# Kernel optimization log

Hardware: AMD Instinct MI355X
Metric: run time of the kernel (lower is better)

The kernel has to match this reference:

```python
import jax, jax.numpy as jnp
import numpy as np

CROP = 14          # initial_crop_size
POOL_K = 2         # maxpool_kernel_size == maxpool_stride


def setup_inputs() -> dict:
    key = jax.random.key(0)
    k1, k2 = jax.random.split(key)
    features = jax.random.normal(k1, (1, 50, 50, 1024), dtype=jnp.float32)
    raw = jax.random.uniform(k2, (1, 300, 4), dtype=jnp.float32)
    # well-formed normalized boxes: y1<=y2, x1<=x2
    ys = jnp.sort(raw[..., 0::2], axis=-1)
    xs = jnp.sort(raw[..., 1::2], axis=-1)
    boxes = jnp.stack([ys[..., 0], xs[..., 0], ys[..., 1], xs[..., 1]], axis=-1)
    return {"features": features, "boxes": boxes}


def _crop_and_resize(feat, boxes, crop_size):
    # feat: [H, W, C]; boxes: [N, 4] normalized (y1, x1, y2, x2)
    # Matches tf.image.crop_and_resize bilinear semantics for crop_size > 1.
    H, W, _ = feat.shape
    y1, x1, y2, x2 = boxes[:, 0], boxes[:, 1], boxes[:, 2], boxes[:, 3]
    grid = jnp.arange(crop_size, dtype=feat.dtype)  # [S]
    # sample coordinates in source pixel space: [N, S]
    ys = y1[:, None] * (H - 1) + grid[None, :] * ((y2 - y1) * (H - 1) / (crop_size - 1))[:, None]
    xs = x1[:, None] * (W - 1) + grid[None, :] * ((x2 - x1) * (W - 1) / (crop_size - 1))[:, None]
    y0f = jnp.floor(ys)
    x0f = jnp.floor(xs)
    wy = (ys - y0f)[:, :, None, None]  # [N, S, 1, 1]
    wx = (xs - x0f)[:, None, :, None]  # [N, 1, S, 1]
    y0 = jnp.clip(y0f.astype(jnp.int32), 0, H - 1)
    y1i = jnp.clip(y0 + 1, 0, H - 1)
    x0 = jnp.clip(x0f.astype(jnp.int32), 0, W - 1)
    x1i = jnp.clip(x0 + 1, 0, W - 1)
    # four corner gathers -> [N, S, S, C]
    tl = feat[y0[:, :, None], x0[:, None, :]]
    tr = feat[y0[:, :, None], x1i[:, None, :]]
    bl = feat[y1i[:, :, None], x0[:, None, :]]
    br = feat[y1i[:, :, None], x1i[:, None, :]]
    top = tl + (tr - tl) * wx
    bot = bl + (br - bl) * wx
    return top + (bot - top) * wy


def reference(features, boxes):
    # features: [1, H, W, C]; boxes: [1, N, 4]
    crops = _crop_and_resize(features[0], boxes[0], CROP)  # [N, 14, 14, C]
    N, S, _, C = crops.shape
    P = S // POOL_K
    # 2x2 stride-2 max pool (kernel == stride, S even)
    pooled = crops.reshape(N, P, POOL_K, P, POOL_K, C).max(axis=(2, 4))  # [N, 7, 7, C]
    return pooled[None]  # [1, N, 7, 7, C]
```

## Files before the change

### kernel.cpp

```cpp
#include <hip/hip_runtime.h>
#include <math.h>

#define FH 50
#define FW 50
#define FC 1024
#define FC4 256
#define NBOX 300
#define PO 7
#define CHQ 4
#define NPIX (FH * FW * FC)
#define BF16_BYTES (NPIX * 2)

typedef float nat4 __attribute__((ext_vector_type(4)));

__device__ __forceinline__ nat4 lerp4(nat4 a, nat4 b, float w) {
    return a + (b - a) * w;
}
__device__ __forceinline__ nat4 max4(nat4 a, nat4 b) {
    nat4 r;
    r.x = fmaxf(a.x, b.x);
    r.y = fmaxf(a.y, b.y);
    r.z = fmaxf(a.z, b.z);
    r.w = fmaxf(a.w, b.w);
    return r;
}
__device__ __forceinline__ nat4 bf2f(uint2 u) {
    nat4 r;
    r.x = __uint_as_float(u.x << 16);
    r.y = __uint_as_float(u.x & 0xffff0000u);
    r.z = __uint_as_float(u.y << 16);
    r.w = __uint_as_float(u.y & 0xffff0000u);
    return r;
}
__device__ __forceinline__ unsigned bfpack(float a, float b) {
    unsigned ua = __float_as_uint(a);
    unsigned ub = __float_as_uint(b);
    ua += 0x7fffu + ((ua >> 16) & 1u);
    ub += 0x7fffu + ((ub >> 16) & 1u);
    return (ua >> 16) | (ub & 0xffff0000u);
}

__global__ __launch_bounds__(256) void cvt_kernel(
    const float* __restrict__ feat, unsigned* __restrict__ ws)
{
    const int i = blockIdx.x * 256 + threadIdx.x;
    const float4 v = reinterpret_cast<const float4*>(feat)[i];
    uint2 w;
    w.x = bfpack(v.x, v.y);
    w.y = bfpack(v.z, v.w);
    reinterpret_cast<uint2*>(ws)[i] = w;
}

template<int NR>
__device__ __forceinline__ void pool_rows(
    const uint2* __restrict__ f2, const int (&rows)[NR], int c,
    float basex, float stepx, float wyA, float wyB,
    nat4* __restrict__ obase)
{
    uint2 cur[NR][2], nxt[NR][2];
    int cc;
    {
        const float xf = floorf(basex);
        cc = min(max((int)xf, 0), FW - 1);
        const int x1 = min(cc + 1, FW - 1);
#pragma unroll
        for (int q = 0; q < NR; ++q) {
            cur[q][0] = f2[(rows[q] + cc) * FC4 + c];
            cur[q][1] = f2[(rows[q] + x1) * FC4 + c];
        }
    }

    nat4 m = (nat4)(-INFINITY);
    for (int ix = 0; ix < 2 * PO; ++ix) {
        int d = 0;
        if (ix < 2 * PO - 1) {
            const float xsn = basex + (float)(ix + 1) * stepx;
            const int nx0 = min(max((int)floorf(xsn), 0), FW - 1);
            const int nx1 = min(nx0 + 1, FW - 1);
            d = nx0 - cc;
            if (d == 1) {
#pragma unroll
                for (int q = 0; q < NR; ++q)
                    nxt[q][1] = f2[(rows[q] + nx1) * FC4 + c];
            } else if (d >= 2) {
#pragma unroll
                for (int q = 0; q < NR; ++q) {
                    nxt[q][0] = f2[(rows[q] + nx0) * FC4 + c];
                    nxt[q][1] = f2[(rows[q] + nx1) * FC4 + c];
                }
            }
            cc = nx0;
        }

        {
            const float xs = basex + (float)ix * stepx;
            const float wx = xs - floorf(xs);
            const nat4 a0 = lerp4(bf2f(cur[0][0]), bf2f(cur[0][1]), wx);
            const nat4 a1 = lerp4(bf2f(cur[1][0]), bf2f(cur[1][1]), wx);
            const nat4 vA = lerp4(a0, a1, wyA);
            nat4 vB;
            if constexpr (NR == 2) {
                vB = lerp4(a0, a1, wyB);
            } else if constexpr (NR == 3) {
                const nat4 a2 = lerp4(bf2f(cur[2][0]), bf2f(cur[2][1]), wx);
                vB = lerp4(a1, a2, wyB);
            } else {
                const nat4 a2 = lerp4(bf2f(cur[2][0]), bf2f(cur[2][1]), wx);
                const nat4 a3 = lerp4(bf2f(cur[3][0]), bf2f(cur[3][1]), wx);
                vB = lerp4(a2, a3, wyB);
            }
            m = max4(m, max4(vA, vB));
        }

        if (ix & 1) {
            __builtin_nontemporal_store(m, obase + (ix >> 1) * FC4);
            m = (nat4)(-INFINITY);
        }

        if (ix < 2 * PO - 1) {
            if (d == 1) {
#pragma unroll
                for (int q = 0; q < NR; ++q) { cur[q][0] = cur[q][1]; cur[q][1] = nxt[q][1]; }
            } else if (d >= 2) {
#pragma unroll
                for (int q = 0; q < NR; ++q) { cur[q][0] = nxt[q][0]; cur[q][1] = nxt[q][1]; }
            }
        }
    }
}

__global__ __launch_bounds__(256) void roi_pool_bf16_kernel(
    const unsigned* __restrict__ ws,
    const float* __restrict__ boxes,
    float* __restrict__ out)
{
    const int j = blockIdx.x & 7;
    const int k = blockIdx.x >> 3;
    const int n = j + 8 * (k / PO);
    if (n >= NBOX) return;
    const int py = k % PO;
    const int c  = threadIdx.x;

    const float by1 = boxes[n * 4 + 0];
    const float bx1 = boxes[n * 4 + 1];
    const float by2 = boxes[n * 4 + 2];
    const float bx2 = boxes[n * 4 + 3];

    const float stepy = (by2 - by1) * (49.0f / 13.0f);
    const float stepx = (bx2 - bx1) * (49.0f / 13.0f);
    const float basey = by1 * 49.0f;
    const float basex = bx1 * 49.0f;

    const float ysA = basey + (float)(2 * py) * stepy;
    const float ysB = ysA + stepy;
    const float fA = floorf(ysA); const float wyA = ysA - fA;
    const float fB = floorf(ysB); const float wyB = ysB - fB;
    const int y0A = min(max((int)fA, 0), FH - 1); const int y1A = min(y0A + 1, FH - 1);
    const int y0B = min(max((int)fB, 0), FH - 1); const int y1B = min(y0B + 1, FH - 1);

    const uint2* __restrict__ f2 = reinterpret_cast<const uint2*>(ws);
    nat4* __restrict__ obase =
        reinterpret_cast<nat4*>(out) + (size_t)(n * (PO * PO) + py * PO) * FC4 + c;

    if (y0B == y0A) {
        const int rows[2] = {y0A * FW, y1A * FW};
        pool_rows<2>(f2, rows, c, basex, stepx, wyA, wyB, obase);
    } else if (y0B == y1A) {
        const int rows[3] = {y0A * FW, y1A * FW, y1B * FW};
        pool_rows<3>(f2, rows, c, basex, stepx, wyA, wyB, obase);
    } else {
        const int rows[4] = {y0A * FW, y1A * FW, y0B * FW, y1B * FW};
        pool_rows<4>(f2, rows, c, basex, stepx, wyA, wyB, obase);
    }
}

__global__ __launch_bounds__(64) void roi_pool_f32_kernel(
    const float* __restrict__ feat,
    const float* __restrict__ boxes,
    float* __restrict__ out)
{
    const int j = blockIdx.x & 7;
    const int k = blockIdx.x >> 3;
    const int n = j + 8 * (k / (PO * CHQ));
    if (n >= NBOX) return;
    const int r  = k % (PO * CHQ);
    const int py = r >> 2;
    const int cq = r & 3;
    const int c4 = cq * 64 + threadIdx.x;

    const float by1 = boxes[n * 4 + 0];
    const float bx1 = boxes[n * 4 + 1];
    const float by2 = boxes[n * 4 + 2];
    const float bx2 = boxes[n * 4 + 3];
    const float stepy = (by2 - by1) * (49.0f / 13.0f);
    const float stepx = (bx2 - bx1) * (49.0f / 13.0f);
    const float basey = by1 * 49.0f;
    const float basex = bx1 * 49.0f;
    const float ysA = basey + (float)(2 * py) * stepy;
    const float ysB = ysA + stepy;
    const float fA = floorf(ysA); const float wyA = ysA - fA;
    const float fB = floorf(ysB); const float wyB = ysB - fB;
    const int y0A = min(max((int)fA, 0), FH - 1); const int y1A = min(y0A + 1, FH - 1);
    const int y0B = min(max((int)fB, 0), FH - 1); const int y1B = min(y0B + 1, FH - 1);

    const nat4* __restrict__ f4 = reinterpret_cast<const nat4*>(feat);
    const int rA0 = y0A * FW, rA1 = y1A * FW, rB0 = y0B * FW, rB1 = y1B * FW;

    int cc = -1000;
    nat4 A00, A01, A10, A11, B00, B01, B10, B11;
    A00 = A01 = A10 = A11 = B00 = B01 = B10 = B11 = (nat4)0.0f;
    nat4 m = (nat4)(-INFINITY);
    nat4* __restrict__ obase =
        reinterpret_cast<nat4*>(out) + (size_t)(n * (PO * PO) + py * PO) * FC4 + c4;

    for (int ix = 0; ix < 2 * PO; ++ix) {
        const float xs = basex + (float)ix * stepx;
        const float xf = floorf(xs);
        const float wx = xs - xf;
        int x0 = min(max((int)xf, 0), FW - 1);
        const int x1 = min(x0 + 1, FW - 1);
        if (x0 != cc) {
            if (x0 == cc + 1) {
                A00 = A01; A10 = A11; B00 = B01; B10 = B11;
                A01 = f4[(rA0 + x1) * FC4 + c4];
                A11 = f4[(rA1 + x1) * FC4 + c4];
                B01 = f4[(rB0 + x1) * FC4 + c4];
                B11 = f4[(rB1 + x1) * FC4 + c4];
            } else {
                A00 = f4[(rA0 + x0) * FC4 + c4];
                A01 = f4[(rA0 + x1) * FC4 + c4];
                A10 = f4[(rA1 + x0) * FC4 + c4];
                A11 = f4[(rA1 + x1) * FC4 + c4];
                B00 = f4[(rB0 + x0) * FC4 + c4];
                B01 = f4[(rB0 + x1) * FC4 + c4];
                B10 = f4[(rB1 + x0) * FC4 + c4];
                B11 = f4[(rB1 + x1) * FC4 + c4];
            }
            cc = x0;
        }
        const nat4 vA = lerp4(lerp4(A00, A01, wx), lerp4(A10, A11, wx), wyA);
        const nat4 vB = lerp4(lerp4(B00, B01, wx), lerp4(B10, B11, wx), wyB);
        m = max4(m, max4(vA, vB));
        if (ix & 1) {
            __builtin_nontemporal_store(m, obase + (ix >> 1) * FC4);
            m = (nat4)(-INFINITY);
        }
    }
}

extern "C" void kernel_launch(void* const* d_in, const int* in_sizes, int n_in,
                              void* d_out, int out_size, void* d_ws, size_t ws_size,
                              hipStream_t stream) {
    (void)in_sizes; (void)n_in; (void)out_size;
    const float* feat  = (const float*)d_in[0];
    const float* boxes = (const float*)d_in[1];
    float* out = (float*)d_out;

    if (ws_size >= (size_t)BF16_BYTES) {
        unsigned* wsb = (unsigned*)d_ws;
        cvt_kernel<<<dim3(NPIX / 4 / 256), dim3(256), 0, stream>>>(feat, wsb);
        roi_pool_bf16_kernel<<<dim3(8 * 38 * PO), dim3(256), 0, stream>>>(wsb, boxes, out);
    } else {
        roi_pool_f32_kernel<<<dim3(8 * 38 * PO * CHQ), dim3(64), 0, stream>>>(feat, boxes, out);
    }
}
```

Before: 98.77 us.

## Split ROI pooling work into channel quarters and x-halves with unrolled loops

The bf16 pooling kernel now runs 64-thread blocks. Each block handles one channel quarter and one half of the output columns (8 or 6 sample columns) for a given box row. The column loop is templated on its length and fully unrolled. The fp32-to-bf16 conversion kernel now uses nontemporal loads. The aim is more, smaller blocks for better latency hiding and load balance. The cost is that the two column halves reload the bilinear corner pixels where they meet, and each block repeats the per-box setup.

```diff
diff --git a/kernel.cpp b/kernel.cpp
--- a/kernel.cpp
+++ b/kernel.cpp
@@ -44,23 +44,25 @@
     const float* __restrict__ feat, unsigned* __restrict__ ws)
 {
     const int i = blockIdx.x * 256 + threadIdx.x;
-    const float4 v = reinterpret_cast<const float4*>(feat)[i];
+    const nat4 v = __builtin_nontemporal_load(
+        reinterpret_cast<const nat4*>(feat) + i);
     uint2 w;
     w.x = bfpack(v.x, v.y);
     w.y = bfpack(v.z, v.w);
     reinterpret_cast<uint2*>(ws)[i] = w;
 }
 
-template<int NR>
+template<int NR, int NIX>
 __device__ __forceinline__ void pool_rows(
-    const uint2* __restrict__ f2, const int (&rows)[NR], int c,
+    const uint2* __restrict__ f2, const int (&rows)[NR], int c, int ix0,
     float basex, float stepx, float wyA, float wyB,
     nat4* __restrict__ obase)
 {
     uint2 cur[NR][2], nxt[NR][2];
     int cc;
     {
-        const float xf = floorf(basex);
+        const float xs0 = basex + (float)ix0 * stepx;
+        const float xf = floorf(xs0);
         cc = min(max((int)xf, 0), FW - 1);
         const int x1 = min(cc + 1, FW - 1);
 #pragma unroll
@@ -71,9 +73,11 @@
     }
 
     nat4 m = (nat4)(-INFINITY);
-    for (int ix = 0; ix < 2 * PO; ++ix) {
+#pragma unroll
+    for (int i = 0; i < NIX; ++i) {
+        const int ix = ix0 + i;
         int d = 0;
-        if (ix < 2 * PO - 1) {
+        if (i < NIX - 1) {
             const float xsn = basex + (float)(ix + 1) * stepx;
             const int nx0 = min(max((int)floorf(xsn), 0), FW - 1);
             const int nx1 = min(nx0 + 1, FW - 1);
@@ -95,20 +99,15 @@
         {
             const float xs = basex + (float)ix * stepx;
             const float wx = xs - floorf(xs);
-            const nat4 a0 = lerp4(bf2f(cur[0][0]), bf2f(cur[0][1]), wx);
-            const nat4 a1 = lerp4(bf2f(cur[1][0]), bf2f(cur[1][1]), wx);
-            const nat4 vA = lerp4(a0, a1, wyA);
+            nat4 a[NR];
+#pragma unroll
+            for (int q = 0; q < NR; ++q)
+                a[q] = lerp4(bf2f(cur[q][0]), bf2f(cur[q][1]), wx);
+            const nat4 vA = lerp4(a[0], a[1], wyA);
             nat4 vB;
-            if constexpr (NR == 2) {
-                vB = lerp4(a0, a1, wyB);
-            } else if constexpr (NR == 3) {
-                const nat4 a2 = lerp4(bf2f(cur[2][0]), bf2f(cur[2][1]), wx);
-                vB = lerp4(a1, a2, wyB);
-            } else {
-                const nat4 a2 = lerp4(bf2f(cur[2][0]), bf2f(cur[2][1]), wx);
-                const nat4 a3 = lerp4(bf2f(cur[3][0]), bf2f(cur[3][1]), wx);
-                vB = lerp4(a2, a3, wyB);
-            }
+            if constexpr (NR == 2)      vB = lerp4(a[0], a[1], wyB);
+            else if constexpr (NR == 3) vB = lerp4(a[1], a[2], wyB);
+            else                        vB = lerp4(a[2], a[3], wyB);
             m = max4(m, max4(vA, vB));
         }
 
@@ -117,7 +116,7 @@
             m = (nat4)(-INFINITY);
         }
 
-        if (ix < 2 * PO - 1) {
+        if (i < NIX - 1) {
             if (d == 1) {
 #pragma unroll
                 for (int q = 0; q < NR; ++q) { cur[q][0] = cur[q][1]; cur[q][1] = nxt[q][1]; }
@@ -129,17 +128,20 @@
     }
 }
 
-__global__ __launch_bounds__(256) void roi_pool_bf16_kernel(
+__global__ __launch_bounds__(64, 6) void roi_pool_bf16_kernel(
     const unsigned* __restrict__ ws,
     const float* __restrict__ boxes,
     float* __restrict__ out)
 {
-    const int j = blockIdx.x & 7;
-    const int k = blockIdx.x >> 3;
-    const int n = j + 8 * (k / PO);
-    if (n >= NBOX) return;
-    const int py = k % PO;
-    const int c  = threadIdx.x;
+    const int j     = blockIdx.x & 7;
+    const int cq    = j & 3;
+    const int g     = blockIdx.x >> 3;
+    const int unit2 = g * 2 + (j >> 2);
+    const int n     = unit2 / 14;
+    const int rem   = unit2 - n * 14;
+    const int py    = rem >> 1;
+    const int s     = rem & 1;
+    const int c     = cq * 64 + threadIdx.x;
 
     const float by1 = boxes[n * 4 + 0];
     const float bx1 = boxes[n * 4 + 1];
@@ -164,13 +166,16 @@
 
     if (y0B == y0A) {
         const int rows[2] = {y0A * FW, y1A * FW};
-        pool_rows<2>(f2, rows, c, basex, stepx, wyA, wyB, obase);
+        if (s == 0) pool_rows<2, 8>(f2, rows, c, 0, basex, stepx, wyA, wyB, obase);
+        else        pool_rows<2, 6>(f2, rows, c, 8, basex, stepx, wyA, wyB, obase);
     } else if (y0B == y1A) {
         const int rows[3] = {y0A * FW, y1A * FW, y1B * FW};
-        pool_rows<3>(f2, rows, c, basex, stepx, wyA, wyB, obase);
+        if (s == 0) pool_rows<3, 8>(f2, rows, c, 0, basex, stepx, wyA, wyB, obase);
+        else        pool_rows<3, 6>(f2, rows, c, 8, basex, stepx, wyA, wyB, obase);
     } else {
         const int rows[4] = {y0A * FW, y1A * FW, y0B * FW, y1B * FW};
-        pool_rows<4>(f2, rows, c, basex, stepx, wyA, wyB, obase);
+        if (s == 0) pool_rows<4, 8>(f2, rows, c, 0, basex, stepx, wyA, wyB, obase);
+        else        pool_rows<4, 6>(f2, rows, c, 8, basex, stepx, wyA, wyB, obase);
     }
 }
 
@@ -259,7 +264,7 @@
     if (ws_size >= (size_t)BF16_BYTES) {
         unsigned* wsb = (unsigned*)d_ws;
         cvt_kernel<<<dim3(NPIX / 4 / 256), dim3(256), 0, stream>>>(feat, wsb);
-        roi_pool_bf16_kernel<<<dim3(8 * 38 * PO), dim3(256), 0, stream>>>(wsb, boxes, out);
+        roi_pool_bf16_kernel<<<dim3(8 * 2100), dim3(64), 0, stream>>>(wsb, boxes, out);
     } else {
         roi_pool_f32_kernel<<<dim3(8 * 38 * PO * CHQ), dim3(64), 0, stream>>>(feat, boxes, out);
     }
```

Measured after the change: 98.09 us. Within noise of the previous version (-0.7%).
